# Performance work log

Hardware: AMD Instinct MI355X
Metric: run time of the kernel (lower is better)

## Reference

```python
import jax, jax.numpy as jnp
import numpy as np

B, S, F_IN, H, NH, NL, HOR = 8, 128, 128, 256, 8, 4, 24


def _ln(x, g, b, eps=1e-5):
    m = jnp.mean(x, axis=-1, keepdims=True)
    v = jnp.var(x, axis=-1, keepdims=True)
    return (x - m) / jnp.sqrt(v + eps) * g + b


def setup_inputs() -> dict:
    key = jax.random.key(0)
    cnt = [0]
    def nrm(shape, scale=0.02):
        cnt[0] += 1
        return jax.random.normal(jax.random.fold_in(key, cnt[0]), shape, jnp.float32) * scale
    d = {}
    d['x'] = jax.random.normal(jax.random.fold_in(key, 999), (B, S, F_IN), jnp.float32)
    # flattened GRN (input F_IN -> hidden H -> output F_IN)
    d['fg_w1'] = nrm((F_IN, H)); d['fg_b1'] = nrm((H,))
    d['fg_w2'] = nrm((H, H));    d['fg_b2'] = nrm((H,))
    d['fg_wo'] = nrm((H, F_IN)); d['fg_bo'] = nrm((F_IN,))
    d['fg_wg'] = nrm((H, F_IN)); d['fg_bg'] = nrm((F_IN,))
    d['fg_sw'] = nrm((F_IN, F_IN)); d['fg_sb'] = nrm((F_IN,))
    d['fg_lng'] = jnp.ones((F_IN,)); d['fg_lnb'] = jnp.zeros((F_IN,))
    # stacked per-variable GRNs (input 1 -> hidden H -> output H), F_IN of them
    d['sv_w1'] = nrm((F_IN, H)); d['sv_b1'] = nrm((F_IN, H))
    d['sv_w2'] = nrm((F_IN, H, H)); d['sv_b2'] = nrm((F_IN, H))
    d['sv_wo'] = nrm((F_IN, H, H)); d['sv_bo'] = nrm((F_IN, H))
    d['sv_wg'] = nrm((F_IN, H, H)); d['sv_bg'] = nrm((F_IN, H))
    d['sv_sw'] = nrm((F_IN, H)); d['sv_sb'] = nrm((F_IN, H))
    d['sv_lng'] = jnp.ones((F_IN, H)); d['sv_lnb'] = jnp.zeros((F_IN, H))
    d['pos_enc'] = nrm((1000, H), 1.0)
    # 2-layer LSTM (torch gate order i,f,g,o)
    for l in (0, 1):
        d[f'l{l}_wih'] = nrm((4 * H, H)); d[f'l{l}_whh'] = nrm((4 * H, H))
        d[f'l{l}_bih'] = nrm((4 * H,));   d[f'l{l}_bhh'] = nrm((4 * H,))
    # NL attention layers, stacked
    d['att_wq'] = nrm((NL, H, H)); d['att_wk'] = nrm((NL, H, H))
    d['att_wv'] = nrm((NL, H, H)); d['att_wo'] = nrm((NL, H, H))
    d['att_bo'] = nrm((NL, H))
    d['att_lng'] = jnp.ones((NL, H)); d['att_lnb'] = jnp.zeros((NL, H))
    # output head and quantile heads
    d['out_w1'] = nrm((H, H // 2)); d['out_b1'] = nrm((H // 2,))
    d['out_w2'] = nrm((H // 2, HOR)); d['out_b2'] = nrm((HOR,))
    d['qw'] = nrm((3, H, HOR)); d['qb'] = nrm((3, HOR))
    return d


def _forward(x, fg_w1, fg_b1, fg_w2, fg_b2, fg_wo, fg_bo, fg_wg, fg_bg, fg_sw, fg_sb,
             fg_lng, fg_lnb, sv_w1, sv_b1, sv_w2, sv_b2, sv_wo, sv_bo, sv_wg, sv_bg,
             sv_sw, sv_sb, sv_lng, sv_lnb, pos_enc, l0_wih, l0_whh, l0_bih, l0_bhh,
             l1_wih, l1_whh, l1_bih, l1_bhh, att_wq, att_wk, att_wv, att_wo, att_bo,
             att_lng, att_lnb, out_w1, out_b1, out_w2, out_b2, qw, qb):
    b, s, f = x.shape
    xf = x.reshape(b * s, f)                      # [N,F]
    # ---- flattened GRN -> variable selection weights ----
    skip = xf @ fg_sw + fg_sb
    h = jax.nn.elu(xf @ fg_w1 + fg_b1)
    h = jax.nn.elu(h @ fg_w2 + fg_b2)
    sw = _ln(jax.nn.sigmoid(h @ fg_wg + fg_bg) * (h @ fg_wo + fg_bo) + skip, fg_lng, fg_lnb)
    sw = jax.nn.softmax(sw, axis=-1)              # [N,F]
    # ---- all per-variable GRNs, batched over the feature axis ----
    h1 = jax.nn.elu(xf[:, :, None] * sv_w1[None] + sv_b1[None])                 # [N,F,H]
    h2 = jax.nn.elu(jnp.einsum('nfh,fhk->nfk', h1, sv_w2) + sv_b2)              # [N,F,H]
    vo = jnp.einsum('nfh,fhk->nfk', h2, sv_wo) + sv_bo
    vg = jax.nn.sigmoid(jnp.einsum('nfh,fhk->nfk', h2, sv_wg) + sv_bg)
    vskip = xf[:, :, None] * sv_sw[None] + sv_sb[None]
    v = _ln(vg * vo + vskip, sv_lng, sv_lnb)                                    # [N,F,H]
    sel = jnp.einsum('nfh,nf->nh', v, sw)                                       # [N,H]
    feats = sel.reshape(b, s, -1) + pos_enc[:s][None]                           # [B,S,H]
    # ---- 2-layer LSTM ----
    def lstm(xseq, wih, whh, bih, bhh):
        hh = whh.shape[1]
        bias = bih + bhh
        def step(carry, xt):
            hp, cp = carry
            g = xt @ wih.T + hp @ whh.T + bias
            i, fg, gg, o = jnp.split(g, 4, axis=-1)
            c = jax.nn.sigmoid(fg) * cp + jax.nn.sigmoid(i) * jnp.tanh(gg)
            hn = jax.nn.sigmoid(o) * jnp.tanh(c)
            return (hn, c), hn
        init = (jnp.zeros((xseq.shape[0], hh), xseq.dtype),
                jnp.zeros((xseq.shape[0], hh), xseq.dtype))
        _, ys = jax.lax.scan(step, init, jnp.swapaxes(xseq, 0, 1))
        return jnp.swapaxes(ys, 0, 1)
    a = lstm(feats, l0_wih, l0_whh, l0_bih, l0_bhh)
    a = lstm(a, l1_wih, l1_whh, l1_bih, l1_bhh)
    # ---- NL self-attention layers ----
    dk = a.shape[-1] // NH
    scale = 1.0 / np.sqrt(dk)
    for l in range(att_wq.shape[0]):
        resid = a
        Q = (a @ att_wq[l]).reshape(b, s, NH, dk)
        K = (a @ att_wk[l]).reshape(b, s, NH, dk)
        V = (a @ att_wv[l]).reshape(b, s, NH, dk)
        scores = jnp.einsum('bqhd,bkhd->bhqk', Q, K) * scale
        w = jax.nn.softmax(scores, axis=-1)
        ctx = jnp.einsum('bhqk,bkhd->bqhd', w, V).reshape(b, s, -1)
        a = _ln(ctx @ att_wo[l] + att_bo[l] + resid, att_lng[l], att_lnb[l])
    gctx = jnp.mean(a, axis=1)                                                  # [B,H]
    pf = jax.nn.relu(gctx @ out_w1 + out_b1) @ out_w2 + out_b2                  # [B,HOR]
    q10 = gctx @ qw[0] + qb[0]
    q50 = gctx @ qw[1] + qb[1]
    q90 = gctx @ qw[2] + qb[2]
    return pf, q10, q50, q90, sw.reshape(b, s, -1), a


def reference(x, fg_w1, fg_b1, fg_w2, fg_b2, fg_wo, fg_bo, fg_wg, fg_bg, fg_sw, fg_sb,
              fg_lng, fg_lnb, sv_w1, sv_b1, sv_w2, sv_b2, sv_wo, sv_bo, sv_wg, sv_bg,
              sv_sw, sv_sb, sv_lng, sv_lnb, pos_enc, l0_wih, l0_whh, l0_bih, l0_bhh,
              l1_wih, l1_whh, l1_bih, l1_bhh, att_wq, att_wk, att_wv, att_wo, att_bo,
              att_lng, att_lnb, out_w1, out_b1, out_w2, out_b2, qw, qb):
    return _forward(x, fg_w1, fg_b1, fg_w2, fg_b2, fg_wo, fg_bo, fg_wg, fg_bg, fg_sw,
                    fg_sb, fg_lng, fg_lnb, sv_w1, sv_b1, sv_w2, sv_b2, sv_wo, sv_bo,
                    sv_wg, sv_bg, sv_sw, sv_sb, sv_lng, sv_lnb, pos_enc, l0_wih, l0_whh,
                    l0_bih, l0_bhh, l1_wih, l1_whh, l1_bih, l1_bhh, att_wq, att_wk,
                    att_wv, att_wo, att_bo, att_lng, att_lnb, out_w1, out_b1, out_w2,
                    out_b2, qw, qb)
```

## Files before the change

kernel.cpp:

```cpp
#include <hip/hip_runtime.h>
#include <cstdint>
#include <cstddef>

typedef __bf16 bf16;
typedef __attribute__((ext_vector_type(4))) __bf16 bf16x4;
typedef __attribute__((ext_vector_type(8))) __bf16 bf16x8;
typedef __attribute__((ext_vector_type(4))) float floatx4;

#define MFMA16(a,b,c) __builtin_amdgcn_mfma_f32_16x16x32_bf16(a,b,c,0,0,0)

__device__ __forceinline__ float sigmf_(float x){ return 1.f/(1.f+expf(-x)); }
__device__ __forceinline__ float eluf_(float x){ return x>0.f ? x : (expf(x)-1.f); }

template<int EPI>
__global__ void __launch_bounds__(256, 2)
gemm_bf16(const float* __restrict__ A, int lda,
          const bf16* __restrict__ BT, int ldb,
          float* __restrict__ C, int ldc,
          const float* __restrict__ b1, const float* __restrict__ b2r,
          int K)
{
  __shared__ char sm[16384 + 8192];
  const int tid = threadIdx.x;
  const int bm = blockIdx.y * 128, bn = blockIdx.x * 64;
  const int l = tid & 63, w = tid >> 6;
  const int wm = (w >> 1) * 64, wn = (w & 1) * 32;
  floatx4 acc[4][2];
  #pragma unroll
  for (int i = 0; i < 4; ++i)
    #pragma unroll
    for (int j = 0; j < 2; ++j)
      #pragma unroll
      for (int r = 0; r < 4; ++r) acc[i][j][r] = 0.f;

  for (int k0 = 0; k0 < K; k0 += 64) {
    {
      int r0 = tid >> 4, kq = (tid & 15) * 4;
      #pragma unroll
      for (int p = 0; p < 8; ++p) {
        int m = r0 + p * 16;
        float4 v = *(const float4*)(A + (size_t)(bm + m) * lda + k0 + kq);
        bf16x4 hv; hv[0]=(bf16)v.x; hv[1]=(bf16)v.y; hv[2]=(bf16)v.z; hv[3]=(bf16)v.w;
        unsigned off = ((unsigned)(m * 128 + kq * 2)) ^ ((unsigned)(m & 7) << 4);
        *(bf16x4*)(sm + off) = hv;
      }
      int n = tid >> 2, c = (tid & 3) * 16;
      const bf16* src = BT + (size_t)(bn + n) * ldb + k0 + c;
      bf16x8 v0 = *(const bf16x8*)(src);
      bf16x8 v1 = *(const bf16x8*)(src + 8);
      unsigned o0 = 16384u + (((unsigned)(n * 128 + c * 2))      ^ ((unsigned)(n & 7) << 4));
      unsigned o1 = 16384u + (((unsigned)(n * 128 + c * 2 + 16)) ^ ((unsigned)(n & 7) << 4));
      *(bf16x8*)(sm + o0) = v0;
      *(bf16x8*)(sm + o1) = v1;
    }
    __syncthreads();
    const int row = l & 15, kb = (l >> 4) * 8;
    #pragma unroll
    for (int kk = 0; kk < 64; kk += 32) {
      bf16x8 a[4], b[2];
      #pragma unroll
      for (int i = 0; i < 4; ++i) {
        int m = wm + i * 16 + row;
        unsigned off = ((unsigned)(m * 128 + (kk + kb) * 2)) ^ ((unsigned)(m & 7) << 4);
        a[i] = *(const bf16x8*)(sm + off);
      }
      #pragma unroll
      for (int j = 0; j < 2; ++j) {
        int n = wn + j * 16 + row;
        unsigned off = 16384u + (((unsigned)(n * 128 + (kk + kb) * 2)) ^ ((unsigned)(n & 7) << 4));
        b[j] = *(const bf16x8*)(sm + off);
      }
      #pragma unroll
      for (int i = 0; i < 4; ++i)
        #pragma unroll
        for (int j = 0; j < 2; ++j)
          acc[i][j] = MFMA16(a[i], b[j], acc[i][j]);
    }
    __syncthreads();
  }
  #pragma unroll
  for (int i = 0; i < 4; ++i)
    #pragma unroll
    for (int j = 0; j < 2; ++j)
      #pragma unroll
      for (int r = 0; r < 4; ++r) {
        int grow = bm + wm + i * 16 + ((l >> 4) << 2) + r;
        int gcol = bn + wn + j * 16 + (l & 15);
        float v = acc[i][j][r];
        if (EPI == 1) v += b1[gcol];
        else if (EPI == 2) { v += b1[gcol]; v = eluf_(v); }
        else if (EPI == 3) { v += (gcol < 128) ? b1[gcol] : b2r[gcol - 128]; }
        else if (EPI == 4) { v += b1[gcol] + b2r[(size_t)grow * ldc + gcol]; }
        C[(size_t)grow * ldc + gcol] = v;
      }
}

__device__ __forceinline__ void tile_tr64(const float* __restrict__ src, int srcld,
                                          bf16* __restrict__ dst, int dstld,
                                          float (*ld)[72])
{
  const int tid = threadIdx.x;
  const int r = tid >> 2, q = tid & 3;
  #pragma unroll
  for (int i = 0; i < 4; ++i) {
    int col = q * 16 + i * 4;
    *(float4*)&ld[r][col] = *(const float4*)(src + (size_t)r * srcld + col);
  }
  __syncthreads();
  bf16x8 o0, o1;
  #pragma unroll
  for (int i = 0; i < 8; ++i) o0[i] = (bf16)ld[q * 16 + i][r];
  #pragma unroll
  for (int i = 0; i < 8; ++i) o1[i] = (bf16)ld[q * 16 + 8 + i][r];
  *(bf16x8*)(dst + (size_t)r * dstld + q * 16) = o0;
  *(bf16x8*)(dst + (size_t)r * dstld + q * 16 + 8) = o1;
}

__global__ void __launch_bounds__(256)
transpose_sv(const float* __restrict__ w2, const float* __restrict__ wo,
             const float* __restrict__ wg, bf16* __restrict__ svT)
{
  __shared__ float ld[64][72];
  int mat = blockIdx.y >> 7;
  int f = blockIdx.y & 127;
  const float* src = (mat == 0 ? w2 : (mat == 1 ? wo : wg)) + (size_t)f * 65536;
  bf16* dst = svT + (size_t)blockIdx.y * 65536;
  int tc = blockIdx.x & 3, tr = blockIdx.x >> 2;
  tile_tr64(src + (size_t)(tr * 64) * 256 + tc * 64, 256,
            dst + (size_t)(tc * 64) * 256 + tr * 64, 256, ld);
}

struct TJob { const float* src; bf16* dst; int R; int C; };
struct TJobs { TJob j[22]; };

__global__ void __launch_bounds__(256)
transpose_misc(TJobs jobs)
{
  __shared__ float ld[64][72];
  TJob J = jobs.j[blockIdx.y];
  int ntc = J.C >> 6;
  int tiles = (J.R >> 6) * ntc;
  if ((int)blockIdx.x >= tiles) return;
  int tc = blockIdx.x % ntc, tr = blockIdx.x / ntc;
  tile_tr64(J.src + (size_t)(tr * 64) * J.C + tc * 64, J.C,
            J.dst + (size_t)(tc * 64) * J.R + tr * 64, J.R, ld);
}

__global__ void __launch_bounds__(256)
cvt4_kernel(const float* __restrict__ s0, const float* __restrict__ s1,
            const float* __restrict__ s2, const float* __restrict__ s3,
            bf16* __restrict__ dst)
{
  size_t i = ((size_t)blockIdx.x * 256 + threadIdx.x) * 4;
  int mat = (int)(i >> 18);
  const float* s = (mat == 0) ? s0 : (mat == 1) ? s1 : (mat == 2) ? s2 : s3;
  float4 v = *(const float4*)(s + (i & 262143));
  bf16x4 o; o[0]=(bf16)v.x; o[1]=(bf16)v.y; o[2]=(bf16)v.z; o[3]=(bf16)v.w;
  *(bf16x4*)(dst + i) = o;
}

__global__ void __launch_bounds__(256, 4)
grnflat_sw_kernel(const float* __restrict__ go, const float* __restrict__ skip,
                  const float* __restrict__ lng, const float* __restrict__ lnb,
                  float* __restrict__ sw_out)
{
  const int tid = threadIdx.x;
  const int m = blockIdx.x * 4 + (tid >> 6);
  const int l = tid & 63, c = l * 2;
  float g0 = go[(size_t)m * 256 + c],       g1 = go[(size_t)m * 256 + c + 1];
  float o0 = go[(size_t)m * 256 + 128 + c], o1 = go[(size_t)m * 256 + 128 + c + 1];
  float sk0 = skip[(size_t)m * 128 + c],    sk1 = skip[(size_t)m * 128 + c + 1];
  float p0 = sigmf_(g0) * o0 + sk0;
  float p1 = sigmf_(g1) * o1 + sk1;
  float s = p0 + p1, s2 = p0 * p0 + p1 * p1;
  #pragma unroll
  for (int k = 1; k < 64; k <<= 1) { s += __shfl_xor(s, k, 64); s2 += __shfl_xor(s2, k, 64); }
  float mean = s * (1.f / 128.f);
  float var = s2 * (1.f / 128.f) - mean * mean;
  float rs = rsqrtf(var + 1e-5f);
  float t0 = (p0 - mean) * rs * lng[c] + lnb[c];
  float t1 = (p1 - mean) * rs * lng[c + 1] + lnb[c + 1];
  float mx = fmaxf(t0, t1);
  #pragma unroll
  for (int k = 1; k < 64; k <<= 1) mx = fmaxf(mx, __shfl_xor(mx, k, 64));
  float e0 = expf(t0 - mx), e1 = expf(t1 - mx);
  float se = e0 + e1;
  #pragma unroll
  for (int k = 1; k < 64; k <<= 1) se += __shfl_xor(se, k, 64);
  float inv = 1.f / se;
  float2 wv; wv.x = e0 * inv; wv.y = e1 * inv;
  *(float2*)(sw_out + (size_t)m * 128 + c) = wv;
}

__global__ void __launch_bounds__(512, 2)
pervar_kernel(const bf16* __restrict__ xT, const bf16* __restrict__ svT,
              const float* __restrict__ w1g, const float* __restrict__ b1g,
              const float* __restrict__ b2g, const float* __restrict__ bog,
              const float* __restrict__ bgg, const float* __restrict__ swg,
              const float* __restrict__ sbg, const float* __restrict__ lngg,
              const float* __restrict__ lnbg,
              bf16* __restrict__ vbuf, int f0)
{
  __shared__ char sm[65536];
  const int tid = threadIdx.x;
  const int fl = blockIdx.y, f = f0 + fl, tile = blockIdx.x;
  const int l = tid & 63, w = tid >> 6;
  const int wm = (w >> 2) * 32, wn = (w & 3) * 64;
  const int row = l & 15, kb = (l >> 4) * 8;
  const size_t fb = (size_t)f * 256;

  {
    int m = tid >> 3, ks8 = (tid & 7) * 32;
    float x = (float)xT[(size_t)f * 1024 + tile * 64 + m];
    #pragma unroll
    for (int i = 0; i < 4; ++i) {
      int k = ks8 + i * 8;
      float4 w0v = *(const float4*)(w1g + fb + k);
      float4 w1v = *(const float4*)(w1g + fb + k + 4);
      float4 b0v = *(const float4*)(b1g + fb + k);
      float4 b1v = *(const float4*)(b1g + fb + k + 4);
      bf16x8 hv;
      hv[0] = (bf16)eluf_(x * w0v.x + b0v.x);
      hv[1] = (bf16)eluf_(x * w0v.y + b0v.y);
      hv[2] = (bf16)eluf_(x * w0v.z + b0v.z);
      hv[3] = (bf16)eluf_(x * w0v.w + b0v.w);
      hv[4] = (bf16)eluf_(x * w1v.x + b1v.x);
      hv[5] = (bf16)eluf_(x * w1v.y + b1v.y);
      hv[6] = (bf16)eluf_(x * w1v.z + b1v.z);
      hv[7] = (bf16)eluf_(x * w1v.w + b1v.w);
      unsigned off = ((unsigned)(m * 512 + k * 2)) ^ ((unsigned)(m & 7) << 4);
      *(bf16x8*)(sm + off) = hv;
    }
  }

  auto stageB = [&](const bf16* BT, int ks) {
    int n = tid >> 1, c = (tid & 1) * 32;
    const bf16* src = BT + (size_t)n * 256 + ks * 64 + c;
    #pragma unroll
    for (int qq = 0; qq < 4; ++qq) {
      unsigned ro = (((unsigned)(n * 128 + (c + qq * 8) * 2)) ^ ((unsigned)(n & 7) << 4));
      *(bf16x8*)(sm + 32768 + ro) = *(const bf16x8*)(src + qq * 8);
    }
  };

  floatx4 acc1[2][4];
  #pragma unroll
  for (int i = 0; i < 2; ++i)
    #pragma unroll
    for (int j = 0; j < 4; ++j)
      #pragma unroll
      for (int r = 0; r < 4; ++r) acc1[i][j][r] = 0.f;
  const bf16* w2T = svT + (size_t)f * 65536;
  for (int ks = 0; ks < 4; ++ks) {
    __syncthreads();
    stageB(w2T, ks);
    __syncthreads();
    #pragma unroll
    for (int kk = 0; kk < 64; kk += 32) {
      int kloc = kk + kb;
      bf16x8 a[2], b[4];
      #pragma unroll
      for (int i = 0; i < 2; ++i) {
        int m = wm + i * 16 + row;
        unsigned off = ((unsigned)(m * 512 + (ks * 64 + kloc) * 2)) ^ ((unsigned)(m & 7) << 4);
        a[i] = *(const bf16x8*)(sm + off);
      }
      #pragma unroll
      for (int j = 0; j < 4; ++j) {
        int n = wn + j * 16 + row;
        unsigned off = 32768u + (((unsigned)(n * 128 + kloc * 2)) ^ ((unsigned)(n & 7) << 4));
        b[j] = *(const bf16x8*)(sm + off);
      }
      #pragma unroll
      for (int i = 0; i < 2; ++i)
        #pragma unroll
        for (int j = 0; j < 4; ++j)
          acc1[i][j] = MFMA16(a[i], b[j], acc1[i][j]);
    }
  }
  __syncthreads();
  #pragma unroll
  for (int i = 0; i < 2; ++i)
    #pragma unroll
    for (int j = 0; j < 4; ++j)
      #pragma unroll
      for (int r = 0; r < 4; ++r) {
        int m = wm + i * 16 + ((l >> 4) << 2) + r;
        int col = wn + j * 16 + (l & 15);
        float v = eluf_(acc1[i][j][r] + b2g[fb + col]);
        unsigned off = ((unsigned)(m * 512 + col * 2)) ^ ((unsigned)(m & 7) << 4);
        *(bf16*)(sm + off) = (bf16)v;
      }
  __syncthreads();

  floatx4 accO[2][4], accG[2][4];
  #pragma unroll
  for (int i = 0; i < 2; ++i)
    #pragma unroll
    for (int j = 0; j < 4; ++j)
      #pragma unroll
      for (int r = 0; r < 4; ++r) { accO[i][j][r] = 0.f; accG[i][j][r] = 0.f; }
  const bf16* woT = svT + ((size_t)128 + f) * 65536;
  const bf16* wgT = svT + ((size_t)256 + f) * 65536;
  for (int ks = 0; ks < 4; ++ks) {
    __syncthreads();
    stageB(woT, ks);
    __syncthreads();
    #pragma unroll
    for (int kk = 0; kk < 64; kk += 32) {
      int kloc = kk + kb;
      bf16x8 a[2], b[4];
      #pragma unroll
      for (int i = 0; i < 2; ++i) {
        int m = wm + i * 16 + row;
        unsigned off = ((unsigned)(m * 512 + (ks * 64 + kloc) * 2)) ^ ((unsigned)(m & 7) << 4);
        a[i] = *(const bf16x8*)(sm + off);
      }
      #pragma unroll
      for (int j = 0; j < 4; ++j) {
        int n = wn + j * 16 + row;
        unsigned off = 32768u + (((unsigned)(n * 128 + kloc * 2)) ^ ((unsigned)(n & 7) << 4));
        b[j] = *(const bf16x8*)(sm + off);
      }
      #pragma unroll
      for (int i = 0; i < 2; ++i)
        #pragma unroll
        for (int j = 0; j < 4; ++j)
          accO[i][j] = MFMA16(a[i], b[j], accO[i][j]);
    }
  }
  for (int ks = 0; ks < 4; ++ks) {
    __syncthreads();
    stageB(wgT, ks);
    __syncthreads();
    #pragma unroll
    for (int kk = 0; kk < 64; kk += 32) {
      int kloc = kk + kb;
      bf16x8 a[2], b[4];
      #pragma unroll
      for (int i = 0; i < 2; ++i) {
        int m = wm + i * 16 + row;
        unsigned off = ((unsigned)(m * 512 + (ks * 64 + kloc) * 2)) ^ ((unsigned)(m & 7) << 4);
        a[i] = *(const bf16x8*)(sm + off);
      }
      #pragma unroll
      for (int j = 0; j < 4; ++j) {
        int n = wn + j * 16 + row;
        unsigned off = 32768u + (((unsigned)(n * 128 + kloc * 2)) ^ ((unsigned)(n & 7) << 4));
        b[j] = *(const bf16x8*)(sm + off);
      }
      #pragma unroll
      for (int i = 0; i < 2; ++i)
        #pragma unroll
        for (int j = 0; j < 4; ++j)
          accG[i][j] = MFMA16(a[i], b[j], accG[i][j]);
    }
  }
  __syncthreads();
  {
    float xm[2][4];
    #pragma unroll
    for (int i = 0; i < 2; ++i)
      #pragma unroll
      for (int r = 0; r < 4; ++r) {
        int m = wm + i * 16 + ((l >> 4) << 2) + r;
        xm[i][r] = (float)xT[(size_t)f * 1024 + tile * 64 + m];
      }
    #pragma unroll
    for (int i = 0; i < 2; ++i)
      #pragma unroll
      for (int j = 0; j < 4; ++j)
        #pragma unroll
        for (int r = 0; r < 4; ++r) {
          int m = wm + i * 16 + ((l >> 4) << 2) + r;
          int col = wn + j * 16 + (l & 15);
          float vg = sigmf_(accG[i][j][r] + bgg[fb + col]);
          float vo = accO[i][j][r] + bog[fb + col];
          float pre = vg * vo + xm[i][r] * swg[fb + col] + sbg[fb + col];
          unsigned off = ((unsigned)(m * 512 + col * 2)) ^ ((unsigned)(m & 7) << 4);
          *(bf16*)(sm + off) = (bf16)pre;
        }
  }
  __syncthreads();
  {
    int m = tid >> 3, q = tid & 7;
    float vals[32];
    float s = 0.f, s2 = 0.f;
    #pragma unroll
    for (int i = 0; i < 4; ++i) {
      unsigned off = ((unsigned)(m * 512 + (q * 32 + i * 8) * 2)) ^ ((unsigned)(m & 7) << 4);
      bf16x8 hv = *(const bf16x8*)(sm + off);
      #pragma unroll
      for (int j = 0; j < 8; ++j) {
        float x = (float)hv[j];
        vals[i * 8 + j] = x; s += x; s2 += x * x;
      }
    }
    s += __shfl_xor(s, 1, 64);  s += __shfl_xor(s, 2, 64);  s += __shfl_xor(s, 4, 64);
    s2 += __shfl_xor(s2, 1, 64); s2 += __shfl_xor(s2, 2, 64); s2 += __shfl_xor(s2, 4, 64);
    float mean = s * (1.f / 256.f);
    float var = s2 * (1.f / 256.f) - mean * mean;
    float rs = rsqrtf(var + 1e-5f);
    bf16* dst = vbuf + ((size_t)fl * 1024 + tile * 64 + m) * 256 + q * 32;
    #pragma unroll
    for (int i = 0; i < 4; ++i) {
      int c = q * 32 + i * 8;
      float4 g0 = *(const float4*)(lngg + fb + c);
      float4 g1 = *(const float4*)(lngg + fb + c + 4);
      float4 bb0 = *(const float4*)(lnbg + fb + c);
      float4 bb1 = *(const float4*)(lnbg + fb + c + 4);
      bf16x8 ov;
      ov[0] = (bf16)((vals[i * 8 + 0] - mean) * rs * g0.x + bb0.x);
      ov[1] = (bf16)((vals[i * 8 + 1] - mean) * rs * g0.y + bb0.y);
      ov[2] = (bf16)((vals[i * 8 + 2] - mean) * rs * g0.z + bb0.z);
      ov[3] = (bf16)((vals[i * 8 + 3] - mean) * rs * g0.w + bb0.w);
      ov[4] = (bf16)((vals[i * 8 + 4] - mean) * rs * g1.x + bb1.x);
      ov[5] = (bf16)((vals[i * 8 + 5] - mean) * rs * g1.y + bb1.y);
      ov[6] = (bf16)((vals[i * 8 + 6] - mean) * rs * g1.z + bb1.z);
      ov[7] = (bf16)((vals[i * 8 + 7] - mean) * rs * g1.w + bb1.w);
      *(bf16x8*)(dst + i * 8) = ov;
    }
  }
}

__global__ void __launch_bounds__(256, 4)
selreduce_kernel(const bf16* __restrict__ vbuf, const float* __restrict__ sw,
                 const float* __restrict__ pos, float* __restrict__ feats,
                 int f0, int FC, int flags)
{
  const int tid = threadIdx.x;
  const int m = blockIdx.x * 4 + (tid >> 6);
  const int hh = (tid & 63) * 4;
  float a0, a1, a2, a3;
  if (flags & 1) { a0 = a1 = a2 = a3 = 0.f; }
  else {
    float4 v = *(const float4*)(feats + (size_t)m * 256 + hh);
    a0 = v.x; a1 = v.y; a2 = v.z; a3 = v.w;
  }
  for (int fi = 0; fi < FC; ++fi) {
    float wgt = sw[(size_t)m * 128 + f0 + fi];
    bf16x4 v = *(const bf16x4*)(vbuf + ((size_t)fi * 1024 + m) * 256 + hh);
    a0 += wgt * (float)v[0]; a1 += wgt * (float)v[1];
    a2 += wgt * (float)v[2]; a3 += wgt * (float)v[3];
  }
  if (flags & 2) {
    float4 p = *(const float4*)(pos + (size_t)(m & 127) * 256 + hh);
    a0 += p.x; a1 += p.y; a2 += p.z; a3 += p.w;
  }
  float4 o; o.x = a0; o.y = a1; o.z = a2; o.w = a3;
  *(float4*)(feats + (size_t)m * 256 + hh) = o;
}

__global__ void __launch_bounds__(256, 1)
lstm_mfma(const bf16* __restrict__ wl, const float* __restrict__ xpre0,
          const float* __restrict__ b0a, const float* __restrict__ b0b,
          const float* __restrict__ b1a, const float* __restrict__ b1b,
          bf16* __restrict__ h0seq, bf16* __restrict__ h1seq,
          float* __restrict__ aseq, unsigned* __restrict__ ctr)
{
  __shared__ float gbuf[4][16][8];
  const int tid = threadIdx.x;
  const int l = tid & 63, w = tid >> 6;
  const int layer = blockIdx.x >> 4, sub = blockIdx.x & 15;
  const int U = sub * 16;
  const int row = w * 256 + U + (l & 15);
  const int ko = (l >> 4) * 8;
  const bf16* whh = wl + (size_t)(layer ? 3 : 1) * 262144 + (size_t)row * 256;
  const bf16* wih1 = wl + (size_t)2 * 262144 + (size_t)row * 256;
  bf16x8 bw[8], bx[8];
  #pragma unroll
  for (int kt = 0; kt < 8; ++kt) bw[kt] = *(const bf16x8*)(whh + kt * 32 + ko);
  if (layer) {
    #pragma unroll
    for (int kt = 0; kt < 8; ++kt) bx[kt] = *(const bf16x8*)(wih1 + kt * 32 + ko);
  }
  const float bsum = layer ? (b1a[row] + b1b[row]) : (b0a[row] + b0b[row]);
  bf16* hs = layer ? h1seq : h0seq;
  unsigned* fown = ctr + (layer ? 512 : 0) + sub * 32;
  float cstate = 0.f;
  const int au = tid >> 3, ab = tid & 7;

  for (int t = 0; t < 128; ++t) {
    float xp[4] = {0.f, 0.f, 0.f, 0.f};
    if (!layer && (l >> 4) < 2) {
      #pragma unroll
      for (int r = 0; r < 4; ++r) {
        int bb = (l >> 4) * 4 + r;
        xp[r] = xpre0[((size_t)((bb << 7) | t)) * 1024 + row];
      }
    }
    if (w == 0) {
      const unsigned* fp = nullptr;
      unsigned tgt = 0;
      if (layer == 0) {
        if (l < 16 && t > 0) { fp = ctr + l * 32; tgt = (unsigned)t; }
      } else {
        if (l < 16) { fp = ctr + l * 32; tgt = (unsigned)(t + 1); }
        else if (l < 32 && t > 0) { fp = ctr + 512 + (l - 16) * 32; tgt = (unsigned)t; }
      }
      if (__any(fp != nullptr)) {
        for (;;) {
          unsigned v = fp ? __hip_atomic_load(fp, __ATOMIC_RELAXED, __HIP_MEMORY_SCOPE_AGENT)
                          : 0xFFFFFFFFu;
          if (__all(v >= tgt)) break;
          __builtin_amdgcn_s_sleep(1);
        }
        if (l == 0) __threadfence();
      }
    }
    __syncthreads();
    floatx4 acc; acc[0] = acc[1] = acc[2] = acc[3] = 0.f;
    if (t > 0) {
      const bf16* hp = hs + (size_t)(t - 1) * 4096 + (size_t)(l & 15) * 256 + ko;
      #pragma unroll
      for (int kt = 0; kt < 8; ++kt)
        acc = MFMA16(*(const bf16x8*)(hp + kt * 32), bw[kt], acc);
    }
    if (layer) {
      const bf16* hp = h0seq + (size_t)t * 4096 + (size_t)(l & 15) * 256 + ko;
      #pragma unroll
      for (int kt = 0; kt < 8; ++kt)
        acc = MFMA16(*(const bf16x8*)(hp + kt * 32), bx[kt], acc);
    }
    if ((l >> 4) < 2) {
      #pragma unroll
      for (int r = 0; r < 4; ++r) {
        int bb = (l >> 4) * 4 + r;
        gbuf[w][l & 15][bb] = acc[r] + bsum + xp[r];
      }
    }
    __syncthreads();
    if (tid < 128) {
      float gi = gbuf[0][au][ab], gf = gbuf[1][au][ab];
      float gg = gbuf[2][au][ab], go = gbuf[3][au][ab];
      cstate = sigmf_(gf) * cstate + sigmf_(gi) * tanhf(gg);
      float h = sigmf_(go) * tanhf(cstate);
      hs[(size_t)t * 4096 + (size_t)ab * 256 + U + au] = (bf16)h;
      if (layer) aseq[((size_t)((ab << 7) | t)) * 256 + U + au] = h;
    }
    __syncthreads();
    if (tid == 0) {
      __threadfence();
      __hip_atomic_store(fown, (unsigned)(t + 1), __ATOMIC_RELEASE, __HIP_MEMORY_SCOPE_AGENT);
    }
  }
}

__global__ void __launch_bounds__(256, 2)
attn_kernel(const float* __restrict__ qkv, float* __restrict__ ctxo)
{
  __shared__ float Kb[128][40];
  __shared__ float Vb[128][40];
  const int tid = threadIdx.x;
  const int b = blockIdx.x >> 3, h = blockIdx.x & 7;
  const int s = tid >> 1, half = tid & 1;
  {
    const float* kr = qkv + ((size_t)(b * 128 + s)) * 768 + 256 + h * 32 + half * 16;
    #pragma unroll
    for (int i = 0; i < 4; ++i) {
      *(float4*)&Kb[s][half * 16 + i * 4] = *(const float4*)(kr + i * 4);
      *(float4*)&Vb[s][half * 16 + i * 4] = *(const float4*)(kr + 256 + i * 4);
    }
  }
  float q[32];
  {
    const float* qr = qkv + ((size_t)(b * 128 + s)) * 768 + h * 32;
    #pragma unroll
    for (int i = 0; i < 8; ++i) {
      float4 v = *(const float4*)(qr + i * 4);
      q[i * 4 + 0] = v.x; q[i * 4 + 1] = v.y; q[i * 4 + 2] = v.z; q[i * 4 + 3] = v.w;
    }
  }
  __syncthreads();
  const float scale = 0.17677669529663687f;
  float se = 0.f;
  float ca[32];
  #pragma unroll
  for (int i = 0; i < 32; ++i) ca[i] = 0.f;
  for (int c0 = 0; c0 < 64; ++c0) {
    int c = half * 64 + c0;
    float d = 0.f;
    #pragma unroll
    for (int i = 0; i < 32; ++i) d += q[i] * Kb[c][i];
    float e = expf(d * scale);
    se += e;
    #pragma unroll
    for (int i = 0; i < 32; ++i) ca[i] += e * Vb[c][i];
  }
  se += __shfl_xor(se, 1, 64);
  #pragma unroll
  for (int i = 0; i < 32; ++i) ca[i] += __shfl_xor(ca[i], 1, 64);
  if (half == 0) {
    float inv = 1.f / se;
    float* outp = ctxo + ((size_t)(b * 128 + s)) * 256 + h * 32;
    #pragma unroll
    for (int i = 0; i < 32; i += 4) {
      float4 v; v.x = ca[i] * inv; v.y = ca[i + 1] * inv; v.z = ca[i + 2] * inv; v.w = ca[i + 3] * inv;
      *(float4*)(outp + i) = v;
    }
  }
}

__global__ void __launch_bounds__(256, 4)
ln_kernel(const float* __restrict__ in, const float* __restrict__ g,
          const float* __restrict__ bta, float* __restrict__ out,
          float* __restrict__ mirror)
{
  const int tid = threadIdx.x;
  const int m = blockIdx.x * 4 + (tid >> 6);
  const int l = tid & 63;
  float4 v = *(const float4*)(in + (size_t)m * 256 + l * 4);
  float s = v.x + v.y + v.z + v.w;
  float s2 = v.x * v.x + v.y * v.y + v.z * v.z + v.w * v.w;
  #pragma unroll
  for (int k = 1; k < 64; k <<= 1) { s += __shfl_xor(s, k, 64); s2 += __shfl_xor(s2, k, 64); }
  float mean = s * (1.f / 256.f);
  float var = s2 * (1.f / 256.f) - mean * mean;
  float rs = rsqrtf(var + 1e-5f);
  float4 gg = *(const float4*)(g + l * 4);
  float4 bb = *(const float4*)(bta + l * 4);
  float4 o;
  o.x = (v.x - mean) * rs * gg.x + bb.x;
  o.y = (v.y - mean) * rs * gg.y + bb.y;
  o.z = (v.z - mean) * rs * gg.z + bb.z;
  o.w = (v.w - mean) * rs * gg.w + bb.w;
  *(float4*)(out + (size_t)m * 256 + l * 4) = o;
  if (mirror) *(float4*)(mirror + (size_t)m * 256 + l * 4) = o;
}

__global__ void __launch_bounds__(256)
gctx_kernel(const float* __restrict__ a, float* __restrict__ g)
{
  int b = blockIdx.x, hh = threadIdx.x;
  float s = 0.f;
  for (int ss = 0; ss < 128; ++ss) s += a[((size_t)b * 128 + ss) * 256 + hh];
  g[b * 256 + hh] = s * (1.f / 128.f);
}

__global__ void __launch_bounds__(256, 1)
head_kernel(const float* __restrict__ g, const float* __restrict__ w1,
            const float* __restrict__ b1, const float* __restrict__ w2,
            const float* __restrict__ b2, const float* __restrict__ qw,
            const float* __restrict__ qb, float* __restrict__ dout)
{
  __shared__ float hid[8][128];
  const int tid = threadIdx.x;
  for (int o = tid; o < 1024; o += 256) {
    int b = o >> 7, j = o & 127;
    float s = b1[j];
    for (int k = 0; k < 256; ++k) s += g[b * 256 + k] * w1[(size_t)k * 128 + j];
    hid[b][j] = s > 0.f ? s : 0.f;
  }
  __syncthreads();
  if (tid < 192) {
    int b = tid / 24, j = tid - b * 24;
    float s = b2[j];
    for (int k = 0; k < 128; ++k) s += hid[b][k] * w2[(size_t)k * 24 + j];
    dout[b * 24 + j] = s;
  }
  for (int o = tid; o < 576; o += 256) {
    int qi = o / 192, rr = o - qi * 192, b = rr / 24, j = rr - b * 24;
    float s = qb[qi * 24 + j];
    for (int k = 0; k < 256; ++k) s += g[b * 256 + k] * qw[((size_t)qi * 256 + k) * 24 + j];
    dout[192 + o] = s;
  }
}

extern "C" void kernel_launch(void* const* d_in, const int* in_sizes, int n_in,
                              void* d_out, int out_size, void* d_ws, size_t ws_size,
                              hipStream_t stream)
{
  (void)in_sizes; (void)n_in; (void)out_size;
  auto F = [&](int i) { return (const float*)d_in[i]; };
  char* ws = (char*)d_ws;
  size_t o = 0;
  auto alloc = [&](size_t b) { size_t r = o; o = (o + b + 255) & ~(size_t)255; return r; };

  size_t svT_o  = alloc((size_t)3 * 128 * 65536 * 2);
  size_t wl_o   = alloc((size_t)4 * 262144 * 2);
  size_t qkvT_o = alloc((size_t)4 * 196608 * 2);
  size_t woT_o  = alloc((size_t)4 * 65536 * 2);
  size_t w1T_o  = alloc(256 * 128 * 2);
  size_t w2T_o  = alloc(256 * 256 * 2);
  size_t goT_o  = alloc(256 * 256 * 2);
  size_t swT_o  = alloc(128 * 128 * 2);
  size_t xT_o   = alloc(128 * 1024 * 2);
  size_t h_o    = alloc((size_t)1024 * 256 * 4);
  size_t h2_o   = alloc((size_t)1024 * 256 * 4);
  size_t go_o   = alloc((size_t)1024 * 256 * 4);
  size_t skip_o = alloc((size_t)1024 * 128 * 4);
  size_t feat_o = alloc((size_t)1024 * 256 * 4);
  size_t xpre_o = alloc((size_t)1024 * 1024 * 4);
  size_t qkv_o  = alloc((size_t)1024 * 768 * 4);
  size_t ctx_o  = alloc((size_t)1024 * 256 * 4);
  size_t pre_o  = alloc((size_t)1024 * 256 * 4);
  size_t aA_o   = alloc((size_t)1024 * 256 * 4);
  size_t aB_o   = alloc((size_t)1024 * 256 * 4);
  size_t gctx_o = alloc(8 * 256 * 4);
  size_t z_o    = alloc((size_t)2 * 1048576 + 4096);
  size_t aseq_o = alloc((size_t)1024 * 256 * 4);
  int FC = 32;
  while (FC > 4 && o + (size_t)FC * 1024 * 256 * 2 > ws_size) FC >>= 1;
  size_t vb_o = alloc((size_t)FC * 1024 * 256 * 2);
  if (o > ws_size) return;

  bf16* svTp  = (bf16*)(ws + svT_o);
  bf16* wlp   = (bf16*)(ws + wl_o);
  bf16* qkvTp = (bf16*)(ws + qkvT_o);
  bf16* woTp  = (bf16*)(ws + woT_o);
  bf16* w1Tp  = (bf16*)(ws + w1T_o);
  bf16* w2Tp  = (bf16*)(ws + w2T_o);
  bf16* goTp  = (bf16*)(ws + goT_o);
  bf16* swTp  = (bf16*)(ws + swT_o);
  bf16* xTp   = (bf16*)(ws + xT_o);
  float* hp    = (float*)(ws + h_o);
  float* h2p   = (float*)(ws + h2_o);
  float* gop   = (float*)(ws + go_o);
  float* skipp = (float*)(ws + skip_o);
  float* featp = (float*)(ws + feat_o);
  float* xprep = (float*)(ws + xpre_o);
  float* qkvp  = (float*)(ws + qkv_o);
  float* ctxp  = (float*)(ws + ctx_o);
  float* prep  = (float*)(ws + pre_o);
  float* aAp   = (float*)(ws + aA_o);
  float* aBp   = (float*)(ws + aB_o);
  float* gctxp = (float*)(ws + gctx_o);
  bf16* h0p    = (bf16*)(ws + z_o);
  bf16* h1p    = (bf16*)(ws + z_o + 1048576);
  unsigned* ctrp = (unsigned*)(ws + z_o + 2097152);
  float* aseqp = (float*)(ws + aseq_o);
  bf16* vbp    = (bf16*)(ws + vb_o);

  float* outp  = (float*)d_out;
  float* sw_do = outp + 768;
  float* a_do  = outp + 131840;

  hipMemsetAsync(ws + z_o, 0, 2097152 + 4096, stream);

  transpose_sv<<<dim3(16, 384), 256, 0, stream>>>(F(15), F(17), F(19), svTp);
  {
    TJobs tj; int nj = 0;
    auto addj = [&](const float* s, bf16* d, int R, int C) { tj.j[nj].src = s; tj.j[nj].dst = d; tj.j[nj].R = R; tj.j[nj].C = C; ++nj; };
    for (int l = 0; l < 4; ++l) {
      addj(F(34) + (size_t)l * 65536, qkvTp + (size_t)l * 196608, 256, 256);
      addj(F(35) + (size_t)l * 65536, qkvTp + (size_t)l * 196608 + 65536, 256, 256);
      addj(F(36) + (size_t)l * 65536, qkvTp + (size_t)l * 196608 + 131072, 256, 256);
      addj(F(37) + (size_t)l * 65536, woTp + (size_t)l * 65536, 256, 256);
    }
    addj(F(1), w1Tp, 128, 256);
    addj(F(3), w2Tp, 256, 256);
    addj(F(7), goTp, 256, 128);
    addj(F(5), goTp + 128 * 256, 256, 128);
    addj(F(9), swTp, 128, 128);
    addj(F(0), xTp, 1024, 128);
    transpose_misc<<<dim3(32, 22), 256, 0, stream>>>(tj);
  }
  cvt4_kernel<<<1024, 256, 0, stream>>>(F(26), F(27), F(30), F(31), wlp);

  auto gemm = [&](int epi, const float* A, int lda, const bf16* BT, int ldb,
                  float* C, int ldc, int M, int N, int K,
                  const float* b1, const float* b2r) {
    dim3 g(N / 64, M / 128);
    switch (epi) {
      case 0: gemm_bf16<0><<<g, 256, 0, stream>>>(A, lda, BT, ldb, C, ldc, b1, b2r, K); break;
      case 1: gemm_bf16<1><<<g, 256, 0, stream>>>(A, lda, BT, ldb, C, ldc, b1, b2r, K); break;
      case 2: gemm_bf16<2><<<g, 256, 0, stream>>>(A, lda, BT, ldb, C, ldc, b1, b2r, K); break;
      case 3: gemm_bf16<3><<<g, 256, 0, stream>>>(A, lda, BT, ldb, C, ldc, b1, b2r, K); break;
      case 4: gemm_bf16<4><<<g, 256, 0, stream>>>(A, lda, BT, ldb, C, ldc, b1, b2r, K); break;
    }
  };

  gemm(2, F(0), 128, w1Tp, 128, hp, 256, 1024, 256, 128, F(2), nullptr);
  gemm(2, hp, 256, w2Tp, 256, h2p, 256, 1024, 256, 256, F(4), nullptr);
  gemm(3, h2p, 256, goTp, 256, gop, 256, 1024, 256, 256, F(8), F(6));
  gemm(1, F(0), 128, swTp, 128, skipp, 128, 1024, 128, 128, F(10), nullptr);
  grnflat_sw_kernel<<<256, 256, 0, stream>>>(gop, skipp, F(11), F(12), sw_do);

  int chunks = 128 / FC;
  for (int c = 0; c < chunks; ++c) {
    pervar_kernel<<<dim3(16, FC), 512, 0, stream>>>(
        xTp, svTp, F(13), F(14), F(16), F(18), F(20), F(21), F(22), F(23), F(24),
        vbp, c * FC);
    selreduce_kernel<<<256, 256, 0, stream>>>(
        vbp, sw_do, F(25), featp, c * FC, FC,
        (c == 0 ? 1 : 0) | (c == chunks - 1 ? 2 : 0));
  }

  gemm(0, featp, 256, wlp, 256, xprep, 1024, 1024, 1024, 256, nullptr, nullptr);
  lstm_mfma<<<32, 256, 0, stream>>>(wlp, xprep, F(28), F(29), F(32), F(33),
                                    h0p, h1p, aseqp, ctrp);

  const float* ain = aseqp;
  float* louts[4] = {aAp, aBp, aAp, aBp};
  for (int l = 0; l < 4; ++l) {
    gemm(0, ain, 256, qkvTp + (size_t)l * 196608, 256, qkvp, 768, 1024, 768, 256, nullptr, nullptr);
    attn_kernel<<<64, 256, 0, stream>>>(qkvp, ctxp);
    gemm(4, ctxp, 256, woTp + (size_t)l * 65536, 256, prep, 256, 1024, 256, 256,
         F(38) + (size_t)l * 256, ain);
    ln_kernel<<<256, 256, 0, stream>>>(prep, F(39) + (size_t)l * 256, F(40) + (size_t)l * 256,
                                       louts[l], l == 3 ? a_do : (float*)nullptr);
    ain = louts[l];
  }

  gctx_kernel<<<8, 256, 0, stream>>>(aBp, gctxp);
  head_kernel<<<1, 256, 0, stream>>>(gctxp, F(41), F(42), F(43), F(44), F(45), F(46), outp);
}
```

Before: 1.146 ms.

## Use relaxed atomic h-state exchange in LSTM recurrence and drop explicit fences

Reworks the persistent LSTM recurrence kernel's cross-block handoff. Hidden-state reads and writes now go through agent-scope relaxed atomics, which removes the __threadfence calls before publishing and after the wait. The gate epilogue now has 64 threads each handle two units, with packed 32-bit bf16 stores. Biases are preloaded once into registers, and the xpre loads are restructured per thread. The aim is to cut per-timestep sync latency on the serial critical path. The risk is memory-ordering correctness, since it relies on release/relaxed semantics without full fences.

```diff
diff --git a/kernel.cpp b/kernel.cpp
--- a/kernel.cpp
+++ b/kernel.cpp
@@ -1,6 +1,7 @@
 #include <hip/hip_runtime.h>
 #include <cstdint>
 #include <cstddef>
+#include <cstring>
 
 typedef __bf16 bf16;
 typedef __attribute__((ext_vector_type(4))) __bf16 bf16x4;
@@ -474,20 +475,34 @@
     #pragma unroll
     for (int kt = 0; kt < 8; ++kt) bx[kt] = *(const bf16x8*)(wih1 + kt * 32 + ko);
   }
-  const float bsum = layer ? (b1a[row] + b1b[row]) : (b0a[row] + b0b[row]);
   bf16* hs = layer ? h1seq : h0seq;
+  const unsigned long long* hsq = (const unsigned long long*)hs;
+  const unsigned long long* h0q = (const unsigned long long*)h0seq;
   unsigned* fown = ctr + (layer ? 512 : 0) + sub * 32;
-  float cstate = 0.f;
-  const int au = tid >> 3, ab = tid & 7;
+  const int ab = tid >> 3, ap = tid & 7;
+  float cs0 = 0.f, cs1 = 0.f;
+  float bs0 = 0.f, bs1 = 0.f, bs2 = 0.f, bs3 = 0.f,
+        bs4 = 0.f, bs5 = 0.f, bs6 = 0.f, bs7 = 0.f;
+  if (tid < 64) {
+    int u0 = U + 2 * ap, u1 = u0 + 1;
+    const float* ba = layer ? b1a : b0a;
+    const float* bb = layer ? b1b : b0b;
+    bs0 = ba[u0] + bb[u0];        bs1 = ba[u1] + bb[u1];
+    bs2 = ba[256 + u0] + bb[256 + u0]; bs3 = ba[256 + u1] + bb[256 + u1];
+    bs4 = ba[512 + u0] + bb[512 + u0]; bs5 = ba[512 + u1] + bb[512 + u1];
+    bs6 = ba[768 + u0] + bb[768 + u0]; bs7 = ba[768 + u1] + bb[768 + u1];
+  }
 
   for (int t = 0; t < 128; ++t) {
-    float xp[4] = {0.f, 0.f, 0.f, 0.f};
-    if (!layer && (l >> 4) < 2) {
-      #pragma unroll
-      for (int r = 0; r < 4; ++r) {
-        int bb = (l >> 4) * 4 + r;
-        xp[r] = xpre0[((size_t)((bb << 7) | t)) * 1024 + row];
-      }
+    float xp0 = 0.f, xp1 = 0.f, xp2 = 0.f, xp3 = 0.f,
+          xp4 = 0.f, xp5 = 0.f, xp6 = 0.f, xp7 = 0.f;
+    if (!layer && tid < 64) {
+      const float* xr = xpre0 + ((size_t)((ab << 7) | t)) * 1024;
+      int u0 = U + 2 * ap;
+      xp0 = xr[u0];        xp1 = xr[u0 + 1];
+      xp2 = xr[256 + u0];  xp3 = xr[256 + u0 + 1];
+      xp4 = xr[512 + u0];  xp5 = xr[512 + u0 + 1];
+      xp6 = xr[768 + u0];  xp7 = xr[768 + u0 + 1];
     }
     if (w == 0) {
       const unsigned* fp = nullptr;
@@ -505,44 +520,76 @@
           if (__all(v >= tgt)) break;
           __builtin_amdgcn_s_sleep(1);
         }
-        if (l == 0) __threadfence();
-      }
-    }
-    __syncthreads();
+      }
+    }
+    __syncthreads();
+    unsigned long long hqA[16], hqB[16];
+    if (t > 0) {
+      size_t e0 = ((size_t)(t - 1) * 4096 + (size_t)(l & 15) * 256 + ko) >> 2;
+      #pragma unroll
+      for (int kt = 0; kt < 8; ++kt) {
+        hqA[2 * kt]     = __hip_atomic_load(hsq + e0 + kt * 8,     __ATOMIC_RELAXED, __HIP_MEMORY_SCOPE_AGENT);
+        hqA[2 * kt + 1] = __hip_atomic_load(hsq + e0 + kt * 8 + 1, __ATOMIC_RELAXED, __HIP_MEMORY_SCOPE_AGENT);
+      }
+    }
+    if (layer) {
+      size_t e1 = ((size_t)t * 4096 + (size_t)(l & 15) * 256 + ko) >> 2;
+      #pragma unroll
+      for (int kt = 0; kt < 8; ++kt) {
+        hqB[2 * kt]     = __hip_atomic_load(h0q + e1 + kt * 8,     __ATOMIC_RELAXED, __HIP_MEMORY_SCOPE_AGENT);
+        hqB[2 * kt + 1] = __hip_atomic_load(h0q + e1 + kt * 8 + 1, __ATOMIC_RELAXED, __HIP_MEMORY_SCOPE_AGENT);
+      }
+    }
     floatx4 acc; acc[0] = acc[1] = acc[2] = acc[3] = 0.f;
     if (t > 0) {
-      const bf16* hp = hs + (size_t)(t - 1) * 4096 + (size_t)(l & 15) * 256 + ko;
-      #pragma unroll
-      for (int kt = 0; kt < 8; ++kt)
-        acc = MFMA16(*(const bf16x8*)(hp + kt * 32), bw[kt], acc);
+      #pragma unroll
+      for (int kt = 0; kt < 8; ++kt) {
+        union { unsigned long long q[2]; bf16x8 v; } u;
+        u.q[0] = hqA[2 * kt]; u.q[1] = hqA[2 * kt + 1];
+        acc = MFMA16(u.v, bw[kt], acc);
+      }
     }
     if (layer) {
-      const bf16* hp = h0seq + (size_t)t * 4096 + (size_t)(l & 15) * 256 + ko;
-      #pragma unroll
-      for (int kt = 0; kt < 8; ++kt)
-        acc = MFMA16(*(const bf16x8*)(hp + kt * 32), bx[kt], acc);
+      #pragma unroll
+      for (int kt = 0; kt < 8; ++kt) {
+        union { unsigned long long q[2]; bf16x8 v; } u;
+        u.q[0] = hqB[2 * kt]; u.q[1] = hqB[2 * kt + 1];
+        acc = MFMA16(u.v, bx[kt], acc);
+      }
     }
     if ((l >> 4) < 2) {
       #pragma unroll
       for (int r = 0; r < 4; ++r) {
         int bb = (l >> 4) * 4 + r;
-        gbuf[w][l & 15][bb] = acc[r] + bsum + xp[r];
-      }
-    }
-    __syncthreads();
-    if (tid < 128) {
-      float gi = gbuf[0][au][ab], gf = gbuf[1][au][ab];
-      float gg = gbuf[2][au][ab], go = gbuf[3][au][ab];
-      cstate = sigmf_(gf) * cstate + sigmf_(gi) * tanhf(gg);
-      float h = sigmf_(go) * tanhf(cstate);
-      hs[(size_t)t * 4096 + (size_t)ab * 256 + U + au] = (bf16)h;
-      if (layer) aseq[((size_t)((ab << 7) | t)) * 256 + U + au] = h;
-    }
-    __syncthreads();
-    if (tid == 0) {
-      __threadfence();
+        gbuf[w][l & 15][bb] = acc[r];
+      }
+    }
+    __syncthreads();
+    if (tid < 64) {
+      int p0 = 2 * ap, p1 = 2 * ap + 1;
+      float gi0 = gbuf[0][p0][ab] + bs0 + xp0, gi1 = gbuf[0][p1][ab] + bs1 + xp1;
+      float gf0 = gbuf[1][p0][ab] + bs2 + xp2, gf1 = gbuf[1][p1][ab] + bs3 + xp3;
+      float gg0 = gbuf[2][p0][ab] + bs4 + xp4, gg1 = gbuf[2][p1][ab] + bs5 + xp5;
+      float go0 = gbuf[3][p0][ab] + bs6 + xp6, go1 = gbuf[3][p1][ab] + bs7 + xp7;
+      cs0 = sigmf_(gf0) * cs0 + sigmf_(gi0) * tanhf(gg0);
+      cs1 = sigmf_(gf1) * cs1 + sigmf_(gi1) * tanhf(gg1);
+      float h0 = sigmf_(go0) * tanhf(cs0);
+      float h1 = sigmf_(go1) * tanhf(cs1);
+      bf16 hb0 = (bf16)h0, hb1 = (bf16)h1;
+      unsigned short q0, q1;
+      __builtin_memcpy(&q0, &hb0, 2);
+      __builtin_memcpy(&q1, &hb1, 2);
+      unsigned pv = (unsigned)q0 | ((unsigned)q1 << 16);
+      unsigned* dst = (unsigned*)(hs + (size_t)t * 4096 + (size_t)ab * 256 + U) + ap;
+      __hip_atomic_store(dst, pv, __ATOMIC_RELAXED, __HIP_MEMORY_SCOPE_AGENT);
+      if (layer) {
+        float2 av; av.x = h0; av.y = h1;
+        *(float2*)(aseq + ((size_t)((ab << 7) | t)) * 256 + U + 2 * ap) = av;
+      }
+    }
+    __syncthreads();
+    if (tid == 0)
       __hip_atomic_store(fown, (unsigned)(t + 1), __ATOMIC_RELEASE, __HIP_MEMORY_SCOPE_AGENT);
-    }
   }
 }
 
```

Result: slower. 1.291 ms (+12.6%).
